# Kernel optimization log

Hardware: AMD Instinct MI355X
Metric: run time of the kernel (lower is better)

Reference implementation:

```python
import jax, jax.numpy as jnp
import numpy as np

HIDDEN = 64
NHEADS = 8
HEAD_DIM = HIDDEN // NHEADS
N_EDGES = 800000
N_NODES = 50000


def setup_inputs() -> dict:
    key = jax.random.key(0)
    k1, k2, k3, k4 = jax.random.split(key, 4)
    keys = jax.random.normal(k1, (N_EDGES, HIDDEN), dtype=jnp.float32)
    queries = jax.random.normal(k2, (N_EDGES, HIDDEN), dtype=jnp.float32)
    values = jax.random.normal(k3, (N_EDGES, HIDDEN), dtype=jnp.float32)
    dst = jax.random.randint(k4, (N_EDGES,), 0, N_NODES, dtype=jnp.int32)
    return {"keys": keys, "queries": queries, "values": values,
            "dst": dst, "num_nodes": N_NODES}


def reference(keys, queries, values, dst, num_nodes):
    E = keys.shape[0]
    temp = HIDDEN ** (-0.5)
    # reshape to (E, H, D) multi-head layout
    k = keys.reshape(E, NHEADS, HEAD_DIM)
    q = queries.reshape(E, NHEADS, HEAD_DIM)
    v = values.reshape(E, NHEADS, HEAD_DIM)
    # edge-wise dot-product score per head, scaled, then LeakyReLU(0.2)
    scores = jnp.sum(k * q, axis=-1) * temp            # (E, H)
    scores = jnp.where(scores >= 0, scores, 0.2 * scores)
    # segment softmax over edges grouped by destination node (dgl.ops.edge_softmax)
    smax = jax.ops.segment_max(scores, dst, num_segments=num_nodes)  # (N, H)
    smax = jnp.where(jnp.isfinite(smax), smax, 0.0)    # nodes with no in-edges
    ex = jnp.exp(scores - smax[dst])                   # (E, H)
    denom = jax.ops.segment_sum(ex, dst, num_segments=num_nodes)    # (N, H)
    weights = ex / denom[dst]                          # (E, H)
    # dropout p=0.0 -> identity; mask/bias are None -> skipped
    weighted = weights[..., None] * v                  # (E, H, D)
    # scatter-sum to destination nodes (dgl.ops.copy_e_sum)
    out = jax.ops.segment_sum(weighted, dst, num_segments=num_nodes)  # (N, H, D)
    return out.reshape(num_nodes, HIDDEN)
```

## Files before the change

### kernel.cpp

```cpp
#include <hip/hip_runtime.h>

#define HIDDEN 64
#define NHEADS 8


__global__ void hist_kernel(const int* __restrict__ dst, int* __restrict__ counts, int E) {
    int i = blockIdx.x * blockDim.x + threadIdx.x;
    if (i < E) atomicAdd(&counts[dst[i]], 1);
}

__global__ void scan1_kernel(const int* __restrict__ counts, int* __restrict__ offsets,
                             int* __restrict__ partials, int N) {
    int tid = threadIdx.x, lane = tid & 63, wid = tid >> 6;
    int i = blockIdx.x * 256 + tid;
    int x0 = (i < N) ? counts[i] : 0;
    int x = x0;
    #pragma unroll
    for (int off = 1; off < 64; off <<= 1) {
        int y = __shfl_up(x, off);
        if (lane >= off) x += y;
    }
    __shared__ int wsum[4];
    if (lane == 63) wsum[wid] = x;
    __syncthreads();
    if (tid == 0) {
        int s = 0;
        #pragma unroll
        for (int w2 = 0; w2 < 4; ++w2) { int t = wsum[w2]; wsum[w2] = s; s += t; }
        partials[blockIdx.x] = s;
    }
    __syncthreads();
    if (i < N) offsets[i] = wsum[wid] + (x - x0);
}

__global__ void scan2_kernel(int* __restrict__ partials, int PB) {
    int tid = threadIdx.x, lane = tid & 63, wid = tid >> 6;
    int x0 = (tid < PB) ? partials[tid] : 0;
    int x = x0;
    #pragma unroll
    for (int off = 1; off < 64; off <<= 1) {
        int y = __shfl_up(x, off);
        if (lane >= off) x += y;
    }
    __shared__ int wsum[4];
    if (lane == 63) wsum[wid] = x;
    __syncthreads();
    if (tid == 0) {
        int s = 0;
        #pragma unroll
        for (int w2 = 0; w2 < 4; ++w2) { int t = wsum[w2]; wsum[w2] = s; s += t; }
    }
    __syncthreads();
    if (tid < PB) partials[tid] = wsum[wid] + (x - x0);
}

__global__ void scan3_kernel(int* __restrict__ offsets, int* __restrict__ cursor,
                             const int* __restrict__ partials, int N, int E) {
    int i = blockIdx.x * 256 + threadIdx.x;
    if (i < N) {
        int o = offsets[i] + partials[blockIdx.x];
        offsets[i] = o;
        cursor[i] = o;
    }
    if (i == 0) offsets[N] = E;
}

__global__ void scatter_kernel(const int* __restrict__ dst, int* __restrict__ cursor,
                               int* __restrict__ edge_ids, int E) {
    int i = blockIdx.x * blockDim.x + threadIdx.x;
    if (i < E) {
        int pos = atomicAdd(&cursor[dst[i]], 1);
        edge_ids[pos] = i;
    }
}

__global__ void gat_gather_kernel(const float* __restrict__ k,
                                  const float* __restrict__ q,
                                  const float* __restrict__ v,
                                  const int* __restrict__ offsets,
                                  const int* __restrict__ edge_ids,
                                  float* __restrict__ out, int N) {
    int wgid = blockIdx.x * (blockDim.x >> 6) + (threadIdx.x >> 6);
    if (wgid >= N) return;
    int lane = threadIdx.x & 63;
    int start = offsets[wgid], end = offsets[wgid + 1];
    int j  = lane >> 3;
    int hs = lane & 7;
    float acc = 0.f, den = 0.f;

    for (int cbase = start; cbase < end; cbase += 8) {
        int e0 = (cbase + 0 < end) ? edge_ids[cbase + 0] : 0;
        int e1 = (cbase + 1 < end) ? edge_ids[cbase + 1] : 0;
        int e2 = (cbase + 2 < end) ? edge_ids[cbase + 2] : 0;
        int e3 = (cbase + 3 < end) ? edge_ids[cbase + 3] : 0;
        int e4 = (cbase + 4 < end) ? edge_ids[cbase + 4] : 0;
        int e5 = (cbase + 5 < end) ? edge_ids[cbase + 5] : 0;
        int e6 = (cbase + 6 < end) ? edge_ids[cbase + 6] : 0;
        int e7 = (cbase + 7 < end) ? edge_ids[cbase + 7] : 0;

        int e = (j < 4) ? ((j < 2) ? (j == 0 ? e0 : e1) : (j == 2 ? e2 : e3))
                        : ((j < 6) ? (j == 4 ? e4 : e5) : (j == 6 ? e6 : e7));

        const float4* kp = (const float4*)(k + (size_t)e * HIDDEN + hs * 8);
        const float4* qp = (const float4*)(q + (size_t)e * HIDDEN + hs * 8);
        float4 k0 = kp[0], k1 = kp[1];
        float4 q0 = qp[0], q1 = qp[1];
        float pr = k0.x * q0.x + k0.y * q0.y + k0.z * q0.z + k0.w * q0.w +
                   k1.x * q1.x + k1.y * q1.y + k1.z * q1.z + k1.w * q1.w;
        float sc = pr * 0.125f;
        sc = (sc >= 0.f) ? sc : 0.2f * sc;
        float exv = (cbase + j < end) ? __expf(sc) : 0.f;

        float w, vv;
        #define GAT_ACC(jj, ej)                                   \
            w = __shfl(exv, (jj) * 8 + (lane >> 3));              \
            vv = v[(size_t)(ej) * HIDDEN + lane];                 \
            acc = fmaf(w, vv, acc);                               \
            den += w;
        GAT_ACC(0, e0) GAT_ACC(1, e1) GAT_ACC(2, e2) GAT_ACC(3, e3)
        GAT_ACC(4, e4) GAT_ACC(5, e5) GAT_ACC(6, e6) GAT_ACC(7, e7)
        #undef GAT_ACC
    }
    out[(size_t)wgid * HIDDEN + lane] = (end > start) ? acc / den : 0.f;
}

extern "C" void kernel_launch(void* const* d_in, const int* in_sizes, int n_in,
                              void* d_out, int out_size, void* d_ws, size_t ws_size,
                              hipStream_t stream) {
    const float* keys    = (const float*)d_in[0];
    const float* queries = (const float*)d_in[1];
    const float* values  = (const float*)d_in[2];
    const int*   dst     = (const int*)d_in[3];
    int E = in_sizes[0] / HIDDEN;
    int N = out_size / HIDDEN;

    int* counts   = (int*)d_ws;
    int* offsets  = counts + N;
    int* cursor   = offsets + N + 1;
    int* partials = cursor + N;
    int* edge_ids = partials + 256;
    float* out    = (float*)d_out;

    hipMemsetAsync(counts, 0, (size_t)N * sizeof(int), stream);

    int threads = 256;
    int eb = (E + threads - 1) / threads;
    int nb256 = (N + 255) / 256;
    hist_kernel<<<eb, threads, 0, stream>>>(dst, counts, E);
    scan1_kernel<<<nb256, 256, 0, stream>>>(counts, offsets, partials, N);
    scan2_kernel<<<1, 256, 0, stream>>>(partials, nb256);
    scan3_kernel<<<nb256, 256, 0, stream>>>(offsets, cursor, partials, N, E);
    scatter_kernel<<<eb, threads, 0, stream>>>(dst, cursor, edge_ids, E);

    int wavesPerBlock = threads / 64;
    int gb = (N + wavesPerBlock - 1) / wavesPerBlock;
    gat_gather_kernel<<<gb, threads, 0, stream>>>(keys, queries, values,
                                                  offsets, edge_ids, out, N);
}
```

Measured before the change: 218.6 us.

## Compute edge scores in scatter pass and store CSR-ordered exp weights

Moves the per-head dot product, LeakyReLU and exp into the scatter kernel, which reads keys and queries in coalesced edge order and writes exp scores into a CSR-ordered buffer. The gather kernel then only reads contiguous weights and gathers values, with a 16-edge unrolled loop for more memory-level parallelism. This trades random k/q gathers for sequential streaming plus an extra weight buffer write/read, and makes the scatter kernel launch 8x more threads.

```diff
diff --git a/kernel.cpp b/kernel.cpp
--- a/kernel.cpp
+++ b/kernel.cpp
@@ -65,63 +65,74 @@
     if (i == 0) offsets[N] = E;
 }
 
-__global__ void scatter_kernel(const int* __restrict__ dst, int* __restrict__ cursor,
-                               int* __restrict__ edge_ids, int E) {
-    int i = blockIdx.x * blockDim.x + threadIdx.x;
-    if (i < E) {
-        int pos = atomicAdd(&cursor[dst[i]], 1);
-        edge_ids[pos] = i;
-    }
+__global__ void scatter_score_kernel(const float* __restrict__ k,
+                                     const float* __restrict__ q,
+                                     const int* __restrict__ dst,
+                                     int* __restrict__ cursor,
+                                     int* __restrict__ edge_ids,
+                                     float* __restrict__ ex8, int E) {
+    int tid = blockIdx.x * blockDim.x + threadIdx.x;
+    int e = tid >> 3, h = tid & 7;
+    if (e >= E) return;
+    int lane = threadIdx.x & 63;
+
+    const float4* kp = (const float4*)(k + (size_t)e * HIDDEN + h * 8);
+    const float4* qp = (const float4*)(q + (size_t)e * HIDDEN + h * 8);
+    float4 k0 = kp[0], k1 = kp[1];
+    float4 q0 = qp[0], q1 = qp[1];
+    float pr = k0.x * q0.x + k0.y * q0.y + k0.z * q0.z + k0.w * q0.w +
+               k1.x * q1.x + k1.y * q1.y + k1.z * q1.z + k1.w * q1.w;
+    float sc = pr * 0.125f;
+    sc = (sc >= 0.f) ? sc : 0.2f * sc;
+    float exv = __expf(sc);
+
+    int pos = 0;
+    if (h == 0) pos = atomicAdd(&cursor[dst[e]], 1);
+    pos = __shfl(pos, lane & ~7);
+    if (h == 0) edge_ids[pos] = e;
+    ex8[(size_t)pos * 8 + h] = exv;
 }
 
-__global__ void gat_gather_kernel(const float* __restrict__ k,
-                                  const float* __restrict__ q,
-                                  const float* __restrict__ v,
+__global__ void gat_gather_kernel(const float* __restrict__ v,
+                                  const float* __restrict__ ex8,
                                   const int* __restrict__ offsets,
                                   const int* __restrict__ edge_ids,
                                   float* __restrict__ out, int N) {
     int wgid = blockIdx.x * (blockDim.x >> 6) + (threadIdx.x >> 6);
     if (wgid >= N) return;
     int lane = threadIdx.x & 63;
+    int h = lane >> 3;
     int start = offsets[wgid], end = offsets[wgid + 1];
-    int j  = lane >> 3;
-    int hs = lane & 7;
+    if (end <= start) {
+        out[(size_t)wgid * HIDDEN + lane] = 0.f;
+        return;
+    }
     float acc = 0.f, den = 0.f;
 
-    for (int cbase = start; cbase < end; cbase += 8) {
-        int e0 = (cbase + 0 < end) ? edge_ids[cbase + 0] : 0;
-        int e1 = (cbase + 1 < end) ? edge_ids[cbase + 1] : 0;
-        int e2 = (cbase + 2 < end) ? edge_ids[cbase + 2] : 0;
-        int e3 = (cbase + 3 < end) ? edge_ids[cbase + 3] : 0;
-        int e4 = (cbase + 4 < end) ? edge_ids[cbase + 4] : 0;
-        int e5 = (cbase + 5 < end) ? edge_ids[cbase + 5] : 0;
-        int e6 = (cbase + 6 < end) ? edge_ids[cbase + 6] : 0;
-        int e7 = (cbase + 7 < end) ? edge_ids[cbase + 7] : 0;
-
-        int e = (j < 4) ? ((j < 2) ? (j == 0 ? e0 : e1) : (j == 2 ? e2 : e3))
-                        : ((j < 6) ? (j == 4 ? e4 : e5) : (j == 6 ? e6 : e7));
-
-        const float4* kp = (const float4*)(k + (size_t)e * HIDDEN + hs * 8);
-        const float4* qp = (const float4*)(q + (size_t)e * HIDDEN + hs * 8);
-        float4 k0 = kp[0], k1 = kp[1];
-        float4 q0 = qp[0], q1 = qp[1];
-        float pr = k0.x * q0.x + k0.y * q0.y + k0.z * q0.z + k0.w * q0.w +
-                   k1.x * q1.x + k1.y * q1.y + k1.z * q1.z + k1.w * q1.w;
-        float sc = pr * 0.125f;
-        sc = (sc >= 0.f) ? sc : 0.2f * sc;
-        float exv = (cbase + j < end) ? __expf(sc) : 0.f;
-
-        float w, vv;
-        #define GAT_ACC(jj, ej)                                   \
-            w = __shfl(exv, (jj) * 8 + (lane >> 3));              \
-            vv = v[(size_t)(ej) * HIDDEN + lane];                 \
-            acc = fmaf(w, vv, acc);                               \
-            den += w;
-        GAT_ACC(0, e0) GAT_ACC(1, e1) GAT_ACC(2, e2) GAT_ACC(3, e3)
-        GAT_ACC(4, e4) GAT_ACC(5, e5) GAT_ACC(6, e6) GAT_ACC(7, e7)
-        #undef GAT_ACC
+    for (int cbase = start; cbase < end; cbase += 16) {
+        int idx[16];
+        int eid[16];
+        float w[16], vv[16];
+        #pragma unroll
+        for (int jj = 0; jj < 16; ++jj) {
+            int i0 = cbase + jj;
+            idx[jj] = (i0 < end) ? i0 : (end - 1);
+        }
+        #pragma unroll
+        for (int jj = 0; jj < 16; ++jj) eid[jj] = edge_ids[idx[jj]];
+        #pragma unroll
+        for (int jj = 0; jj < 16; ++jj) {
+            w[jj]  = ex8[(size_t)idx[jj] * 8 + h];
+            vv[jj] = v[(size_t)eid[jj] * HIDDEN + lane];
+        }
+        #pragma unroll
+        for (int jj = 0; jj < 16; ++jj) {
+            float m = (cbase + jj < end) ? w[jj] : 0.f;
+            acc = fmaf(m, vv[jj], acc);
+            den += m;
+        }
     }
-    out[(size_t)wgid * HIDDEN + lane] = (end > start) ? acc / den : 0.f;
+    out[(size_t)wgid * HIDDEN + lane] = acc / den;
 }
 
 extern "C" void kernel_launch(void* const* d_in, const int* in_sizes, int n_in,
@@ -139,6 +150,7 @@
     int* cursor   = offsets + N + 1;
     int* partials = cursor + N;
     int* edge_ids = partials + 256;
+    float* ex8    = (float*)(edge_ids + E);
     float* out    = (float*)d_out;
 
     hipMemsetAsync(counts, 0, (size_t)N * sizeof(int), stream);
@@ -150,10 +162,13 @@
     scan1_kernel<<<nb256, 256, 0, stream>>>(counts, offsets, partials, N);
     scan2_kernel<<<1, 256, 0, stream>>>(partials, nb256);
     scan3_kernel<<<nb256, 256, 0, stream>>>(offsets, cursor, partials, N, E);
-    scatter_kernel<<<eb, threads, 0, stream>>>(dst, cursor, edge_ids, E);
+
+    int ehb = ((E * NHEADS) + threads - 1) / threads;
+    scatter_score_kernel<<<ehb, threads, 0, stream>>>(keys, queries, dst,
+                                                      cursor, edge_ids, ex8, E);
 
     int wavesPerBlock = threads / 64;
     int gb = (N + wavesPerBlock - 1) / wavesPerBlock;
-    gat_gather_kernel<<<gb, threads, 0, stream>>>(keys, queries, values,
-                                                  offsets, edge_ids, out, N);
+    gat_gather_kernel<<<gb, threads, 0, stream>>>(values, ex8, offsets,
+                                                  edge_ids, out, N);
 }
```

Result: faster. 207.5 us (-5.1%).
